# Kernel tuning notes

Measured on AMD Instinct MI355X. Metric: run time of the kernel, lower is better.

The kernel has to match this reference:

```python
import jax, jax.numpy as jnp
import numpy as np

EMBED, NH, NKV, HD, FF, EPS = 2048, 16, 4, 128, 5632, 1e-5
B, S = 2, 2048

def rmsnorm(x, w):
    xf = x.astype(jnp.float32)
    n = xf * jax.lax.rsqrt(jnp.mean(xf * xf, axis=-1, keepdims=True) + EPS)
    return n.astype(x.dtype) * w

def apply_rope(x, freqs_cis):
    # x: (b, s, h, d); freqs_cis: (s, d//2, 2)
    b, s, h, d = x.shape
    xr = x.astype(jnp.float32).reshape(b, s, h, d // 2, 2)
    f = freqs_cis.reshape(1, s, 1, d // 2, 2)
    out = jnp.stack([xr[..., 0] * f[..., 0] - xr[..., 1] * f[..., 1],
                     xr[..., 1] * f[..., 0] + xr[..., 0] * f[..., 1]], axis=-1)
    return out.reshape(b, s, h, d).astype(x.dtype)

def setup_inputs() -> dict:
    key = jax.random.key(0)
    ks = jax.random.split(key, 8)
    x = jax.random.normal(ks[0], (B, S, EMBED), dtype=jnp.float32)
    attention_mask = jnp.tril(jnp.ones((S, S), dtype=jnp.int32))[None].repeat(B, axis=0)
    # RoPE cos/sin table
    inv = 1.0 / (10000.0 ** (np.arange(0, HD, 2, dtype=np.float32) / HD))
    t = np.arange(S, dtype=np.float32)[:, None] * inv[None, :]  # (S, HD//2)
    freqs_cis = jnp.asarray(np.stack([np.cos(t), np.sin(t)], axis=-1))  # (S, HD//2, 2)
    input_pos = jnp.arange(S, dtype=jnp.int32)
    sd = 0.02
    w_qkv = jax.random.normal(ks[1], ((NH + 2 * NKV) * HD, EMBED), dtype=jnp.float32) * sd
    w_fc = jax.random.normal(ks[2], (EMBED, EMBED), dtype=jnp.float32) * sd
    w1 = jax.random.normal(ks[3], (FF, EMBED), dtype=jnp.float32) * sd
    w2 = jax.random.normal(ks[4], (FF, EMBED), dtype=jnp.float32) * sd
    w3 = jax.random.normal(ks[5], (EMBED, FF), dtype=jnp.float32) * sd
    attn_norm_w = jnp.ones((EMBED,), dtype=jnp.float32)
    ff_norm_w = jnp.ones((EMBED,), dtype=jnp.float32)
    return {"x": x, "attention_mask": attention_mask, "freqs_cis": freqs_cis,
            "input_pos": input_pos, "w_qkv": w_qkv, "w_fc": w_fc,
            "w1": w1, "w2": w2, "w3": w3,
            "attn_norm_w": attn_norm_w, "ff_norm_w": ff_norm_w}

def reference(x, attention_mask, freqs_cis, input_pos, w_qkv, w_fc, w1, w2, w3, attn_norm_w, ff_norm_w):
    b, s, _ = x.shape
    n_rep = NH // NKV
    # --- attention block ---
    h = rmsnorm(x, attn_norm_w)
    qkv = h @ w_qkv.T
    q, k, v = jnp.split(qkv, [NH * HD, NH * HD + NKV * HD], axis=-1)
    q = q.reshape(b, s, NH, HD)
    k = k.reshape(b, s, NKV, HD)
    v = v.reshape(b, s, NKV, HD)
    q = apply_rope(q, freqs_cis)
    k = apply_rope(k, freqs_cis)
    q = q.transpose(0, 2, 1, 3)                       # (b, NH, s, d)
    k = jnp.repeat(k.transpose(0, 2, 1, 3), n_rep, axis=1)  # (b, NH, s, d)
    v = jnp.repeat(v.transpose(0, 2, 1, 3), n_rep, axis=1)
    scale = 1.0 / jnp.sqrt(jnp.float32(EMBED))  # NOTE: source scales by sqrt(embedding_dim)
    scores = jnp.einsum('bhqd,bhkd->bhqk', q, k) * scale
    scores = jnp.where(attention_mask[:, None] == 0, -jnp.inf, scores)
    probs = jax.nn.softmax(scores, axis=-1)
    attn = jnp.einsum('bhqk,bhkd->bhqd', probs, v)
    attn = attn.transpose(0, 2, 1, 3).reshape(b, s, EMBED) @ w_fc.T
    h = x + attn
    # --- SwiGLU FFN ---
    g = rmsnorm(h, ff_norm_w)
    ff = (jax.nn.silu(g @ w1.T) * (g @ w2.T)) @ w3.T
    return h + ff
```

## Files before the change

### kernel.cpp

```cpp
#include <hip/hip_runtime.h>
#include <cstdint>
#include <cstddef>

typedef unsigned short u16;
typedef short bf16x8 __attribute__((ext_vector_type(8)));
typedef float f32x4 __attribute__((ext_vector_type(4)));

#define AS1C(p) ((const __attribute__((address_space(1))) void*)(p))
#define AS3(p)  ((__attribute__((address_space(3))) void*)(p))
#define MFMA_BF16 __builtin_amdgcn_mfma_f32_16x16x32_bf16

__device__ __forceinline__ u16 f2bf(float f) {
    union { float f; unsigned int u; } v; v.f = f;
    unsigned int r = v.u + 0x7fffu + ((v.u >> 16) & 1u);
    return (u16)(r >> 16);
}

struct U16x4 { u16 x, y, z, w; };

__global__ __launch_bounds__(256) void cvt_kernel(const float* __restrict__ src,
                                                  u16* __restrict__ dst, int n4) {
    int i = blockIdx.x * 256 + threadIdx.x;
    if (i < n4) {
        const float4 v = ((const float4*)src)[i];
        U16x4 o; o.x = f2bf(v.x); o.y = f2bf(v.y); o.z = f2bf(v.z); o.w = f2bf(v.w);
        ((U16x4*)dst)[i] = o;
    }
}

__global__ __launch_bounds__(256) void rmsnorm_kernel(const float* __restrict__ X,
                                                      const float* __restrict__ W,
                                                      u16* __restrict__ Out) {
    const int row = blockIdx.x;
    const int t = threadIdx.x;
    const float* xr = X + (size_t)row * 2048;
    float4 a = ((const float4*)xr)[2 * t];
    float4 b = ((const float4*)xr)[2 * t + 1];
    float ss = a.x*a.x + a.y*a.y + a.z*a.z + a.w*a.w
             + b.x*b.x + b.y*b.y + b.z*b.z + b.w*b.w;
    #pragma unroll
    for (int off = 1; off < 64; off <<= 1) ss += __shfl_xor(ss, off);
    __shared__ float red[4];
    if ((t & 63) == 0) red[t >> 6] = ss;
    __syncthreads();
    float tot = red[0] + red[1] + red[2] + red[3];
    float rs = rsqrtf(tot * (1.0f / 2048.0f) + 1e-5f);
    float vals[8] = {a.x, a.y, a.z, a.w, b.x, b.y, b.z, b.w};
    const int base = t * 8;
    u16* orow = Out + (size_t)row * 2048 + base;
    #pragma unroll
    for (int j = 0; j < 8; ++j) orow[j] = f2bf(vals[j] * rs * W[base + j]);
}

__global__ __launch_bounds__(256) void rope_kernel(const float* __restrict__ qkv,
                                                   const float* __restrict__ fr,
                                                   u16* __restrict__ Qo, u16* __restrict__ Ko,
                                                   u16* __restrict__ Vo) {
    const int tok = blockIdx.x;
    const int b = tok >> 11, s = tok & 2047;
    const int t = threadIdx.x;
    const float* row = qkv + (size_t)tok * 3072;
    const float* f = fr + (size_t)s * 128;
    #pragma unroll
    for (int i = 0; i < 4; ++i) {
        int p = t + i * 256;
        int h = p >> 6, pi = p & 63;
        float x0 = row[h * 128 + pi * 2];
        float x1 = row[h * 128 + pi * 2 + 1];
        float c = f[pi * 2], sn = f[pi * 2 + 1];
        size_t ob = ((size_t)(b * 16 + h) * 2048 + s) * 128 + pi * 2;
        Qo[ob]     = f2bf(x0 * c - x1 * sn);
        Qo[ob + 1] = f2bf(x1 * c + x0 * sn);
    }
    {
        int kh = t >> 6, pi = t & 63;
        float x0 = row[2048 + kh * 128 + pi * 2];
        float x1 = row[2048 + kh * 128 + pi * 2 + 1];
        float c = f[pi * 2], sn = f[pi * 2 + 1];
        size_t ob = ((size_t)(b * 4 + kh) * 2048 + s) * 128 + pi * 2;
        Ko[ob]     = f2bf(x0 * c - x1 * sn);
        Ko[ob + 1] = f2bf(x1 * c + x0 * sn);
    }
    #pragma unroll
    for (int i = 0; i < 2; ++i) {
        int e = t + i * 256;
        int kh = e >> 7, d = e & 127;
        Vo[((size_t)(b * 4 + kh) * 128 + d) * 2048 + s] = f2bf(row[2560 + e]);
    }
}

template <bool RESID, bool DUAL>
__global__ __launch_bounds__(256, 2) void gemm_bt(
    const u16* __restrict__ A, const u16* __restrict__ B0, const u16* __restrict__ B1,
    const float* __restrict__ RES, float* __restrict__ Cf, u16* __restrict__ Cb,
    int M, int N, int K) {
    __shared__ __align__(16) u16 As[128 * 32];
    __shared__ __align__(16) u16 Bs[128 * 32];
    __shared__ __align__(16) u16 Bs2[128 * 32];
    const int w = threadIdx.x >> 6;
    const int lane = threadIdx.x & 63;
    const int bm = blockIdx.y * 128;
    const int bn = blockIdx.x * 128;
    const int wm = (w >> 1) * 64;
    const int wn = (w & 1) * 64;
    const int lr = lane & 15;
    const int kq = (lane >> 4) * 8;
    const int srow = lane >> 2;
    const int skc = (lane & 3) * 8;
    f32x4 acc[4][4];
    f32x4 acc2[4][4];
    const f32x4 z = {0.f, 0.f, 0.f, 0.f};
    #pragma unroll
    for (int i = 0; i < 4; ++i)
        #pragma unroll
        for (int j = 0; j < 4; ++j) { acc[i][j] = z; acc2[i][j] = z; }

    for (int k0 = 0; k0 < K; k0 += 32) {
        #pragma unroll
        for (int c = 0; c < 2; ++c) {
            const int chunk = 2 * w + c;
            const int r = chunk * 16 + srow;
            const int lofs = chunk * 512 + lane * 8;
            __builtin_amdgcn_global_load_lds(AS1C(A + (size_t)(bm + r) * K + k0 + skc),
                                             AS3(&As[lofs]), 16, 0, 0);
            __builtin_amdgcn_global_load_lds(AS1C(B0 + (size_t)(bn + r) * K + k0 + skc),
                                             AS3(&Bs[lofs]), 16, 0, 0);
            if constexpr (DUAL)
                __builtin_amdgcn_global_load_lds(AS1C(B1 + (size_t)(bn + r) * K + k0 + skc),
                                                 AS3(&Bs2[lofs]), 16, 0, 0);
        }
        __syncthreads();
        bf16x8 af[4], bfr[4];
        #pragma unroll
        for (int tm = 0; tm < 4; ++tm) af[tm] = *(const bf16x8*)&As[(wm + tm * 16 + lr) * 32 + kq];
        #pragma unroll
        for (int tn = 0; tn < 4; ++tn) bfr[tn] = *(const bf16x8*)&Bs[(wn + tn * 16 + lr) * 32 + kq];
        #pragma unroll
        for (int tm = 0; tm < 4; ++tm)
            #pragma unroll
            for (int tn = 0; tn < 4; ++tn)
                acc[tm][tn] = MFMA_BF16(af[tm], bfr[tn], acc[tm][tn], 0, 0, 0);
        if constexpr (DUAL) {
            #pragma unroll
            for (int tn = 0; tn < 4; ++tn) bfr[tn] = *(const bf16x8*)&Bs2[(wn + tn * 16 + lr) * 32 + kq];
            #pragma unroll
            for (int tm = 0; tm < 4; ++tm)
                #pragma unroll
                for (int tn = 0; tn < 4; ++tn)
                    acc2[tm][tn] = MFMA_BF16(af[tm], bfr[tn], acc2[tm][tn], 0, 0, 0);
        }
        __syncthreads();
    }
    #pragma unroll
    for (int tm = 0; tm < 4; ++tm) {
        const int row0 = bm + wm + tm * 16 + (lane >> 4) * 4;
        #pragma unroll
        for (int tn = 0; tn < 4; ++tn) {
            const int col = bn + wn + tn * 16 + (lane & 15);
            #pragma unroll
            for (int r = 0; r < 4; ++r) {
                const size_t idx = (size_t)(row0 + r) * N + col;
                if constexpr (DUAL) {
                    float aa = acc[tm][tn][r];
                    float bb = acc2[tm][tn][r];
                    float sg = aa / (1.0f + __expf(-aa));
                    Cb[idx] = f2bf(sg * bb);
                } else {
                    float v = acc[tm][tn][r];
                    if constexpr (RESID) v += RES[idx];
                    Cf[idx] = v;
                }
            }
        }
    }
}

__global__ __launch_bounds__(256, 2) void attn_kernel(
    const u16* __restrict__ Q, const u16* __restrict__ Kg,
    const u16* __restrict__ Vt, u16* __restrict__ O) {
    __shared__ __align__(16) u16 Ks[32 * 128];
    __shared__ __align__(16) u16 Vs[128 * 32];
    __shared__ __align__(16) u16 Ps[4][16 * 32];
    const int qt = blockIdx.x, h = blockIdx.y, b = blockIdx.z;
    const int kvh = h >> 2;
    const int w = threadIdx.x >> 6, lane = threadIdx.x & 63;
    const int q0 = qt * 64;
    const int qw = q0 + w * 16;
    const int lr = lane & 15;
    const int quad = lane >> 4;
    const int srow = lane >> 2, skc = (lane & 3) * 8;
    const u16* qbase = Q + (((size_t)(b * 16 + h) * 2048) + qw + lr) * 128;
    bf16x8 qf[4];
    #pragma unroll
    for (int kk = 0; kk < 4; ++kk) qf[kk] = *(const bf16x8*)(qbase + kk * 32 + quad * 8);
    f32x4 o[8];
    const f32x4 z = {0.f, 0.f, 0.f, 0.f};
    #pragma unroll
    for (int i = 0; i < 8; ++i) o[i] = z;
    float m_r[4] = {-1e30f, -1e30f, -1e30f, -1e30f};
    float l_r[4] = {0.f, 0.f, 0.f, 0.f};
    const float scale = 0.022097086912079608f;
    const float LOG2E = 1.4426950408889634f;
    const int nkt = (q0 + 64) >> 5;
    const u16* kgbase = Kg + (size_t)(b * 4 + kvh) * 2048 * 128;
    const u16* vgbase = Vt + (size_t)(b * 4 + kvh) * 128 * 2048;

    for (int kt = 0; kt < nkt; ++kt) {
        __syncthreads();
        #pragma unroll
        for (int c = 0; c < 2; ++c) {
            const int chunk = 2 * w + c;
            const int lofs = chunk * 512 + lane * 8;
            __builtin_amdgcn_global_load_lds(AS1C(kgbase + (size_t)kt * 32 * 128 + lofs),
                                             AS3(&Ks[lofs]), 16, 0, 0);
            const int d_ = chunk * 16 + srow;
            __builtin_amdgcn_global_load_lds(AS1C(vgbase + (size_t)d_ * 2048 + kt * 32 + skc),
                                             AS3(&Vs[lofs]), 16, 0, 0);
        }
        __syncthreads();
        if (kt * 32 <= qw + 15) {
            f32x4 s0 = z, s1 = z;
            #pragma unroll
            for (int kk = 0; kk < 4; ++kk) {
                bf16x8 k0f = *(const bf16x8*)&Ks[lr * 128 + kk * 32 + quad * 8];
                bf16x8 k1f = *(const bf16x8*)&Ks[(16 + lr) * 128 + kk * 32 + quad * 8];
                s0 = MFMA_BF16(qf[kk], k0f, s0, 0, 0, 0);
                s1 = MFMA_BF16(qf[kk], k1f, s1, 0, 0, 0);
            }
            float p0[4], p1[4], mt[4];
            #pragma unroll
            for (int r = 0; r < 4; ++r) {
                int rg = qw + quad * 4 + r;
                int cg = kt * 32 + lr;
                float v0 = s0[r] * scale;
                float v1 = s1[r] * scale;
                if (cg > rg) v0 = -1e30f;
                if (cg + 16 > rg) v1 = -1e30f;
                p0[r] = v0; p1[r] = v1;
                mt[r] = fmaxf(v0, v1);
            }
            #pragma unroll
            for (int off = 1; off < 16; off <<= 1)
                #pragma unroll
                for (int r = 0; r < 4; ++r) mt[r] = fmaxf(mt[r], __shfl_xor(mt[r], off));
            float alpha[4], rsum[4];
            #pragma unroll
            for (int r = 0; r < 4; ++r) {
                float mn = fmaxf(m_r[r], mt[r]);
                alpha[r] = exp2f((m_r[r] - mn) * LOG2E);
                m_r[r] = mn;
                p0[r] = exp2f((p0[r] - mn) * LOG2E);
                p1[r] = exp2f((p1[r] - mn) * LOG2E);
                rsum[r] = p0[r] + p1[r];
            }
            #pragma unroll
            for (int off = 1; off < 16; off <<= 1)
                #pragma unroll
                for (int r = 0; r < 4; ++r) rsum[r] += __shfl_xor(rsum[r], off);
            #pragma unroll
            for (int r = 0; r < 4; ++r) l_r[r] = l_r[r] * alpha[r] + rsum[r];
            #pragma unroll
            for (int dt = 0; dt < 8; ++dt)
                #pragma unroll
                for (int r = 0; r < 4; ++r) o[dt][r] *= alpha[r];
            u16* pw = &Ps[w][0];
            #pragma unroll
            for (int r = 0; r < 4; ++r) {
                pw[(quad * 4 + r) * 32 + lr]      = f2bf(p0[r]);
                pw[(quad * 4 + r) * 32 + 16 + lr] = f2bf(p1[r]);
            }
            bf16x8 pf = *(const bf16x8*)&pw[lr * 32 + quad * 8];
            #pragma unroll
            for (int dt = 0; dt < 8; ++dt) {
                bf16x8 vf = *(const bf16x8*)&Vs[(dt * 16 + lr) * 32 + quad * 8];
                o[dt] = MFMA_BF16(pf, vf, o[dt], 0, 0, 0);
            }
        }
    }
    float inv[4];
    #pragma unroll
    for (int r = 0; r < 4; ++r) inv[r] = 1.0f / l_r[r];
    #pragma unroll
    for (int dt = 0; dt < 8; ++dt)
        #pragma unroll
        for (int r = 0; r < 4; ++r) {
            int rg = qw + quad * 4 + r;
            size_t idx = ((size_t)b * 2048 + rg) * 2048 + h * 128 + dt * 16 + lr;
            O[idx] = f2bf(o[dt][r] * inv[r]);
        }
}

extern "C" void kernel_launch(void* const* d_in, const int* in_sizes, int n_in,
                              void* d_out, int out_size, void* d_ws, size_t ws_size,
                              hipStream_t stream) {
    (void)in_sizes; (void)n_in; (void)out_size; (void)ws_size;
    const float* x    = (const float*)d_in[0];
    const float* fr   = (const float*)d_in[2];
    const float* wqkv = (const float*)d_in[4];
    const float* wfc  = (const float*)d_in[5];
    const float* w1   = (const float*)d_in[6];
    const float* w2   = (const float*)d_in[7];
    const float* w3   = (const float*)d_in[8];
    const float* anw  = (const float*)d_in[9];
    const float* fnw  = (const float*)d_in[10];
    float* out = (float*)d_out;
    char* ws = (char*)d_ws;
    size_t off = 0;
    auto alloc = [&](size_t bytes) -> void* {
        void* p = ws + off;
        off += (bytes + 255) & ~(size_t)255;
        return p;
    };
    u16*   wqkv_b = (u16*)alloc((size_t)3072 * 2048 * 2);
    u16*   wfc_b  = (u16*)alloc((size_t)2048 * 2048 * 2);
    u16*   w1_b   = (u16*)alloc((size_t)5632 * 2048 * 2);
    u16*   w2_b   = (u16*)alloc((size_t)5632 * 2048 * 2);
    u16*   w3_b   = (u16*)alloc((size_t)2048 * 5632 * 2);
    u16*   xn_b   = (u16*)alloc((size_t)4096 * 2048 * 2);
    float* qkv_f  = (float*)alloc((size_t)4096 * 3072 * 4);
    u16*   q_b    = (u16*)alloc((size_t)4096 * 2048 * 2);
    u16*   k_b    = (u16*)alloc((size_t)4096 * 512 * 2);
    u16*   vt_b   = (u16*)alloc((size_t)4096 * 512 * 2);
    float* h_f    = (float*)alloc((size_t)4096 * 2048 * 4);
    u16* attn_b = xn_b;
    u16* t_b    = (u16*)qkv_f;
    u16* g_b    = q_b;

    cvt_kernel<<<6144, 256, 0, stream>>>(wqkv, wqkv_b, 3072 * 2048 / 4);
    cvt_kernel<<<4096, 256, 0, stream>>>(wfc, wfc_b, 2048 * 2048 / 4);
    cvt_kernel<<<11264, 256, 0, stream>>>(w1, w1_b, 5632 * 2048 / 4);
    cvt_kernel<<<11264, 256, 0, stream>>>(w2, w2_b, 5632 * 2048 / 4);
    cvt_kernel<<<11264, 256, 0, stream>>>(w3, w3_b, 2048 * 5632 / 4);

    rmsnorm_kernel<<<4096, 256, 0, stream>>>(x, anw, xn_b);
    gemm_bt<false, false><<<dim3(24, 32), 256, 0, stream>>>(
        xn_b, wqkv_b, nullptr, nullptr, qkv_f, nullptr, 4096, 3072, 2048);
    rope_kernel<<<4096, 256, 0, stream>>>(qkv_f, fr, q_b, k_b, vt_b);
    attn_kernel<<<dim3(32, 16, 2), 256, 0, stream>>>(q_b, k_b, vt_b, attn_b);
    gemm_bt<true, false><<<dim3(16, 32), 256, 0, stream>>>(
        attn_b, wfc_b, nullptr, x, h_f, nullptr, 4096, 2048, 2048);
    rmsnorm_kernel<<<4096, 256, 0, stream>>>(h_f, fnw, g_b);
    gemm_bt<false, true><<<dim3(44, 32), 256, 0, stream>>>(
        g_b, w1_b, w2_b, nullptr, nullptr, t_b, 4096, 5632, 2048);
    gemm_bt<true, false><<<dim3(16, 32), 256, 0, stream>>>(
        t_b, w3_b, nullptr, h_f, out, nullptr, 4096, 2048, 5632);
}
```

Baseline: 1.058 ms.

## Enlarge attention tiles to 128 queries by 64 keys with reversed block order

```diff
diff --git a/kernel.cpp b/kernel.cpp
--- a/kernel.cpp
+++ b/kernel.cpp
@@ -178,116 +178,154 @@
 __global__ __launch_bounds__(256, 2) void attn_kernel(
     const u16* __restrict__ Q, const u16* __restrict__ Kg,
     const u16* __restrict__ Vt, u16* __restrict__ O) {
-    __shared__ __align__(16) u16 Ks[32 * 128];
-    __shared__ __align__(16) u16 Vs[128 * 32];
-    __shared__ __align__(16) u16 Ps[4][16 * 32];
-    const int qt = blockIdx.x, h = blockIdx.y, b = blockIdx.z;
+    __shared__ __align__(16) u16 Ks[16 * 512];
+    __shared__ __align__(16) u16 Vs[16 * 512];
+    __shared__ __align__(16) u16 Ps[4][32 * 72];
+    const int qt = (int)gridDim.x - 1 - (int)blockIdx.x;
+    const int h = blockIdx.y, b = blockIdx.z;
     const int kvh = h >> 2;
     const int w = threadIdx.x >> 6, lane = threadIdx.x & 63;
-    const int q0 = qt * 64;
-    const int qw = q0 + w * 16;
-    const int lr = lane & 15;
-    const int quad = lane >> 4;
-    const int srow = lane >> 2, skc = (lane & 3) * 8;
-    const u16* qbase = Q + (((size_t)(b * 16 + h) * 2048) + qw + lr) * 128;
-    bf16x8 qf[4];
-    #pragma unroll
-    for (int kk = 0; kk < 4; ++kk) qf[kk] = *(const bf16x8*)(qbase + kk * 32 + quad * 8);
-    f32x4 o[8];
+    const int lr = lane & 15, quad = lane >> 4;
+    const int q0 = qt * 128;
+    const int wq = q0 + w * 32;
+    const u16* kgbase = Kg + (size_t)(b * 4 + kvh) * 2048 * 128;
+    const u16* vgbase = Vt + (size_t)(b * 4 + kvh) * 128 * 2048;
+    bf16x8 qf[2][4];
+    #pragma unroll
+    for (int mt = 0; mt < 2; ++mt)
+        #pragma unroll
+        for (int kk = 0; kk < 4; ++kk)
+            qf[mt][kk] = *(const bf16x8*)(Q + ((size_t)(b * 16 + h) * 2048 + wq + mt * 16 + lr) * 128
+                                          + kk * 32 + quad * 8);
+    f32x4 o[2][8];
     const f32x4 z = {0.f, 0.f, 0.f, 0.f};
     #pragma unroll
-    for (int i = 0; i < 8; ++i) o[i] = z;
-    float m_r[4] = {-1e30f, -1e30f, -1e30f, -1e30f};
-    float l_r[4] = {0.f, 0.f, 0.f, 0.f};
+    for (int mt = 0; mt < 2; ++mt)
+        #pragma unroll
+        for (int dt = 0; dt < 8; ++dt) o[mt][dt] = z;
+    float m_r[2][4], l_r[2][4];
+    #pragma unroll
+    for (int mt = 0; mt < 2; ++mt)
+        #pragma unroll
+        for (int r = 0; r < 4; ++r) { m_r[mt][r] = -1e30f; l_r[mt][r] = 0.f; }
     const float scale = 0.022097086912079608f;
     const float LOG2E = 1.4426950408889634f;
-    const int nkt = (q0 + 64) >> 5;
-    const u16* kgbase = Kg + (size_t)(b * 4 + kvh) * 2048 * 128;
-    const u16* vgbase = Vt + (size_t)(b * 4 + kvh) * 128 * 2048;
+    const int nkt = (q0 + 128) >> 6;
 
     for (int kt = 0; kt < nkt; ++kt) {
         __syncthreads();
         #pragma unroll
-        for (int c = 0; c < 2; ++c) {
-            const int chunk = 2 * w + c;
-            const int lofs = chunk * 512 + lane * 8;
-            __builtin_amdgcn_global_load_lds(AS1C(kgbase + (size_t)kt * 32 * 128 + lofs),
-                                             AS3(&Ks[lofs]), 16, 0, 0);
-            const int d_ = chunk * 16 + srow;
-            __builtin_amdgcn_global_load_lds(AS1C(vgbase + (size_t)d_ * 2048 + kt * 32 + skc),
-                                             AS3(&Vs[lofs]), 16, 0, 0);
+        for (int c = 0; c < 4; ++c) {
+            const int i = w * 4 + c;
+            __builtin_amdgcn_global_load_lds(
+                AS1C(kgbase + (size_t)(kt * 64 + lane) * 128 + i * 8),
+                AS3(&Ks[i * 512 + lane * 8]), 16, 0, 0);
+            __builtin_amdgcn_global_load_lds(
+                AS1C(vgbase + (size_t)((i & 1) * 64 + lane) * 2048 + kt * 64 + (i >> 1) * 8),
+                AS3(&Vs[i * 512 + lane * 8]), 16, 0, 0);
         }
         __syncthreads();
-        if (kt * 32 <= qw + 15) {
-            f32x4 s0 = z, s1 = z;
+        if (kt * 64 <= wq + 31) {
+            f32x4 s[2][4];
+            #pragma unroll
+            for (int mt = 0; mt < 2; ++mt)
+                #pragma unroll
+                for (int nt = 0; nt < 4; ++nt) s[mt][nt] = z;
             #pragma unroll
             for (int kk = 0; kk < 4; ++kk) {
-                bf16x8 k0f = *(const bf16x8*)&Ks[lr * 128 + kk * 32 + quad * 8];
-                bf16x8 k1f = *(const bf16x8*)&Ks[(16 + lr) * 128 + kk * 32 + quad * 8];
-                s0 = MFMA_BF16(qf[kk], k0f, s0, 0, 0, 0);
-                s1 = MFMA_BF16(qf[kk], k1f, s1, 0, 0, 0);
-            }
-            float p0[4], p1[4], mt[4];
+                bf16x8 kf[4];
+                #pragma unroll
+                for (int nt = 0; nt < 4; ++nt)
+                    kf[nt] = *(const bf16x8*)&Ks[(kk * 4 + quad) * 512 + (nt * 16 + lr) * 8];
+                #pragma unroll
+                for (int mt = 0; mt < 2; ++mt)
+                    #pragma unroll
+                    for (int nt = 0; nt < 4; ++nt)
+                        s[mt][nt] = MFMA_BF16(qf[mt][kk], kf[nt], s[mt][nt], 0, 0, 0);
+            }
+            u16* pw = &Ps[w][0];
+            #pragma unroll
+            for (int mt = 0; mt < 2; ++mt) {
+                float mx[4];
+                #pragma unroll
+                for (int r = 0; r < 4; ++r) {
+                    const int rg = wq + mt * 16 + quad * 4 + r;
+                    float mm = -1e30f;
+                    #pragma unroll
+                    for (int nt = 0; nt < 4; ++nt) {
+                        const int cg = kt * 64 + nt * 16 + lr;
+                        float v = s[mt][nt][r] * scale;
+                        if (cg > rg) v = -1e30f;
+                        s[mt][nt][r] = v;
+                        mm = fmaxf(mm, v);
+                    }
+                    mx[r] = mm;
+                }
+                #pragma unroll
+                for (int off = 1; off < 16; off <<= 1)
+                    #pragma unroll
+                    for (int r = 0; r < 4; ++r) mx[r] = fmaxf(mx[r], __shfl_xor(mx[r], off));
+                float rsum[4];
+                #pragma unroll
+                for (int r = 0; r < 4; ++r) {
+                    const float mn = fmaxf(m_r[mt][r], mx[r]);
+                    const float alpha = exp2f((m_r[mt][r] - mn) * LOG2E);
+                    m_r[mt][r] = mn;
+                    float rs = 0.f;
+                    #pragma unroll
+                    for (int nt = 0; nt < 4; ++nt) {
+                        float p = exp2f((s[mt][nt][r] - mn) * LOG2E);
+                        s[mt][nt][r] = p;
+                        rs += p;
+                    }
+                    rsum[r] = rs;
+                    l_r[mt][r] *= alpha;
+                    #pragma unroll
+                    for (int dt = 0; dt < 8; ++dt) o[mt][dt][r] *= alpha;
+                }
+                #pragma unroll
+                for (int off = 1; off < 16; off <<= 1)
+                    #pragma unroll
+                    for (int r = 0; r < 4; ++r) rsum[r] += __shfl_xor(rsum[r], off);
+                #pragma unroll
+                for (int r = 0; r < 4; ++r) l_r[mt][r] += rsum[r];
+                #pragma unroll
+                for (int nt = 0; nt < 4; ++nt)
+                    #pragma unroll
+                    for (int r = 0; r < 4; ++r)
+                        pw[(mt * 16 + quad * 4 + r) * 72 + nt * 16 + lr] = f2bf(s[mt][nt][r]);
+            }
+            #pragma unroll
+            for (int kf = 0; kf < 2; ++kf) {
+                bf16x8 pf[2];
+                #pragma unroll
+                for (int mt = 0; mt < 2; ++mt)
+                    pf[mt] = *(const bf16x8*)&pw[(mt * 16 + lr) * 72 + kf * 32 + quad * 8];
+                #pragma unroll
+                for (int dt = 0; dt < 8; ++dt) {
+                    bf16x8 vf = *(const bf16x8*)&Vs[((kf * 4 + quad) * 2 + (dt >> 2)) * 512
+                                                    + ((dt & 3) * 16 + lr) * 8];
+                    #pragma unroll
+                    for (int mt = 0; mt < 2; ++mt)
+                        o[mt][dt] = MFMA_BF16(pf[mt], vf, o[mt][dt], 0, 0, 0);
+                }
+            }
+        }
+    }
+    #pragma unroll
+    for (int mt = 0; mt < 2; ++mt) {
+        float inv[4];
+        #pragma unroll
+        for (int r = 0; r < 4; ++r) inv[r] = 1.0f / l_r[mt][r];
+        #pragma unroll
+        for (int dt = 0; dt < 8; ++dt)
             #pragma unroll
             for (int r = 0; r < 4; ++r) {
-                int rg = qw + quad * 4 + r;
-                int cg = kt * 32 + lr;
-                float v0 = s0[r] * scale;
-                float v1 = s1[r] * scale;
-                if (cg > rg) v0 = -1e30f;
-                if (cg + 16 > rg) v1 = -1e30f;
-                p0[r] = v0; p1[r] = v1;
-                mt[r] = fmaxf(v0, v1);
-            }
-            #pragma unroll
-            for (int off = 1; off < 16; off <<= 1)
-                #pragma unroll
-                for (int r = 0; r < 4; ++r) mt[r] = fmaxf(mt[r], __shfl_xor(mt[r], off));
-            float alpha[4], rsum[4];
-            #pragma unroll
-            for (int r = 0; r < 4; ++r) {
-                float mn = fmaxf(m_r[r], mt[r]);
-                alpha[r] = exp2f((m_r[r] - mn) * LOG2E);
-                m_r[r] = mn;
-                p0[r] = exp2f((p0[r] - mn) * LOG2E);
-                p1[r] = exp2f((p1[r] - mn) * LOG2E);
-                rsum[r] = p0[r] + p1[r];
-            }
-            #pragma unroll
-            for (int off = 1; off < 16; off <<= 1)
-                #pragma unroll
-                for (int r = 0; r < 4; ++r) rsum[r] += __shfl_xor(rsum[r], off);
-            #pragma unroll
-            for (int r = 0; r < 4; ++r) l_r[r] = l_r[r] * alpha[r] + rsum[r];
-            #pragma unroll
-            for (int dt = 0; dt < 8; ++dt)
-                #pragma unroll
-                for (int r = 0; r < 4; ++r) o[dt][r] *= alpha[r];
-            u16* pw = &Ps[w][0];
-            #pragma unroll
-            for (int r = 0; r < 4; ++r) {
-                pw[(quad * 4 + r) * 32 + lr]      = f2bf(p0[r]);
-                pw[(quad * 4 + r) * 32 + 16 + lr] = f2bf(p1[r]);
-            }
-            bf16x8 pf = *(const bf16x8*)&pw[lr * 32 + quad * 8];
-            #pragma unroll
-            for (int dt = 0; dt < 8; ++dt) {
-                bf16x8 vf = *(const bf16x8*)&Vs[(dt * 16 + lr) * 32 + quad * 8];
-                o[dt] = MFMA_BF16(pf, vf, o[dt], 0, 0, 0);
-            }
-        }
-    }
-    float inv[4];
-    #pragma unroll
-    for (int r = 0; r < 4; ++r) inv[r] = 1.0f / l_r[r];
-    #pragma unroll
-    for (int dt = 0; dt < 8; ++dt)
-        #pragma unroll
-        for (int r = 0; r < 4; ++r) {
-            int rg = qw + quad * 4 + r;
-            size_t idx = ((size_t)b * 2048 + rg) * 2048 + h * 128 + dt * 16 + lr;
-            O[idx] = f2bf(o[dt][r] * inv[r]);
-        }
+                const int rg = wq + mt * 16 + quad * 4 + r;
+                const size_t idx = ((size_t)b * 2048 + rg) * 2048 + h * 128 + dt * 16 + lr;
+                O[idx] = f2bf(o[mt][dt][r] * inv[r]);
+            }
+    }
 }
 
 extern "C" void kernel_launch(void* const* d_in, const int* in_sizes, int n_in,
@@ -336,7 +374,7 @@
     gemm_bt<false, false><<<dim3(24, 32), 256, 0, stream>>>(
         xn_b, wqkv_b, nullptr, nullptr, qkv_f, nullptr, 4096, 3072, 2048);
     rope_kernel<<<4096, 256, 0, stream>>>(qkv_f, fr, q_b, k_b, vt_b);
-    attn_kernel<<<dim3(32, 16, 2), 256, 0, stream>>>(q_b, k_b, vt_b, attn_b);
+    attn_kernel<<<dim3(16, 16, 2), 256, 0, stream>>>(q_b, k_b, vt_b, attn_b);
     gemm_bt<true, false><<<dim3(16, 32), 256, 0, stream>>>(
         attn_b, wfc_b, nullptr, x, h_f, nullptr, 4096, 2048, 2048);
     rmsnorm_kernel<<<4096, 256, 0, stream>>>(h_f, fnw, g_b);
```

Result: faster. 933.6 us (-11.8%).
